# Kernel optimization log

Measured on AMD Instinct MI355X. Metric: run time of the kernel, lower is better.

The kernel has to match this reference:

```python
import jax, jax.numpy as jnp
import numpy as np

N, E, D, H, L = 20000, 320000, 256, 8, 2
C = D // H  # out_channels per head = 32
NEG_SLOPE = 0.2
LN_EPS = 1e-5


def setup_inputs() -> dict:
    key = jax.random.key(0)
    ks = jax.random.split(key, 12)
    s = 0.05
    return {
        "x": jax.random.normal(ks[0], (N, D), jnp.float32),
        "edge_index": jax.random.randint(ks[1], (2, E), 0, N, dtype=jnp.int32),
        "edge_attr": jax.random.uniform(ks[2], (E, 1), jnp.float32),
        "Wl": jax.random.normal(ks[3], (L, D, D), jnp.float32) * s,   # lin_l weight (source)
        "bl": jnp.zeros((L, D), jnp.float32),
        "Wr": jax.random.normal(ks[4], (L, D, D), jnp.float32) * s,   # lin_r weight (target)
        "br": jnp.zeros((L, D), jnp.float32),
        "We": jax.random.normal(ks[5], (L, 1, D), jnp.float32) * s,   # lin_edge (edge_dim=1)
        "att": jax.random.normal(ks[6], (L, H, C), jnp.float32) * s,  # attention vector a
        "bias_out": jnp.zeros((L, D), jnp.float32),                   # GATv2 output bias
        "ln_g": jnp.ones((L, D), jnp.float32),
        "ln_b": jnp.zeros((L, D), jnp.float32),
    }


def _gatv2_layer(x, src, dst, edge_attr, Wl, bl, Wr, br, We, att, bias_out):
    # dense transforms: [N, H, C]
    xl = (x @ Wl + bl).reshape(N, H, C)  # source features (x_j)
    xr = (x @ Wr + br).reshape(N, H, C)  # target features (x_i)
    ea = (edge_attr @ We).reshape(E, H, C)
    # GATv2 scoring: a^T LeakyReLU(W_l x_j + W_r x_i + W_e e_ij)
    m = jax.nn.leaky_relu(xl[src] + xr[dst] + ea, NEG_SLOPE)  # [E, H, C]
    logits = jnp.einsum('ehc,hc->eh', m, att)                 # [E, H]
    # scatter-softmax over incoming edges of each destination node
    mx = jax.ops.segment_max(logits, dst, num_segments=N)     # [N, H]
    ex = jnp.exp(logits - mx[dst])
    den = jax.ops.segment_sum(ex, dst, num_segments=N)        # [N, H]
    alpha = ex / (den[dst] + 1e-16)                           # [E, H]
    # weighted aggregation of source messages
    out = jax.ops.segment_sum(xl[src] * alpha[:, :, None], dst, num_segments=N)
    return out.reshape(N, D) + bias_out


def _layernorm(h, g, b):
    mu = jnp.mean(h, axis=-1, keepdims=True)
    var = jnp.mean(jnp.square(h - mu), axis=-1, keepdims=True)
    return (h - mu) * jax.lax.rsqrt(var + LN_EPS) * g + b


def reference(x, edge_index, edge_attr, Wl, bl, Wr, br, We, att, bias_out, ln_g, ln_b):
    src, dst = edge_index[0], edge_index[1]
    for i in range(L):
        h = _gatv2_layer(x, src, dst, edge_attr, Wl[i], bl[i], Wr[i], br[i],
                         We[i], att[i], bias_out[i])
        h = jax.nn.elu(_layernorm(h, ln_g[i], ln_b[i]))
        x = x + h  # residual (dropout = identity in reference)
    return x
```

## Files before the change

### kernel.cpp

```cpp
#include <hip/hip_runtime.h>
#include <hip/hip_bf16.h>
#include <math.h>

#define Nn 20000
#define Ee 320000
#define Dd 256
#define Hh 8
#define Cc 32
#define NEG_SLOPE 0.2f
#define LN_EPS 1e-5f

typedef __bf16 bf16x8 __attribute__((ext_vector_type(8)));
typedef float f32x4 __attribute__((ext_vector_type(4)));

__device__ __forceinline__ unsigned f2bf_rn(float f) {
    unsigned u = __float_as_uint(f);
    return (u + 0x7fffu + ((u >> 16) & 1u)) >> 16;
}


__global__ void count_kernel(const int* __restrict__ ei, int* __restrict__ counts) {
    int e = blockIdx.x * 256 + threadIdx.x;
    if (e < Ee) atomicAdd(&counts[ei[Ee + e]], 1);
}

__global__ void __launch_bounds__(1024) scan_kernel(
        const int* __restrict__ counts, int* __restrict__ offs, int* __restrict__ gctr) {
    __shared__ int buf[1024];
    __shared__ int bbase;
    int tid = threadIdx.x;
    int i = blockIdx.x * 1024 + tid;
    int v = (i < Nn) ? counts[i] : 0;
    buf[tid] = v;
    __syncthreads();
    for (int off = 1; off < 1024; off <<= 1) {
        int t = (tid >= off) ? buf[tid - off] : 0;
        __syncthreads();
        buf[tid] += t;
        __syncthreads();
    }
    int incl = buf[tid];
    if (tid == 1023) bbase = atomicAdd(gctr, incl);
    __syncthreads();
    if (i < Nn) offs[i] = bbase + incl - v;
}

__global__ void fill_kernel(const int* __restrict__ ei, const float* __restrict__ eattr,
                            const int* __restrict__ offs,
                            int* __restrict__ cursor, int2* __restrict__ csr_meta) {
    int e = blockIdx.x * 256 + threadIdx.x;
    if (e < Ee) {
        int d = ei[Ee + e];
        int p = atomicAdd(&cursor[d], 1);
        int2 m;
        m.x = ei[e];
        m.y = __float_as_int(eattr[e]);
        csr_meta[offs[d] + p] = m;
    }
}


__global__ void cast_x_kernel(const float* __restrict__ x, unsigned short* __restrict__ Xb) {
    int i = blockIdx.x * 256 + threadIdx.x;
    float4 v = ((const float4*)x)[i];
    uint2 pk;
    pk.x = f2bf_rn(v.x) | (f2bf_rn(v.y) << 16);
    pk.y = f2bf_rn(v.z) | (f2bf_rn(v.w) << 16);
    ((uint2*)Xb)[i] = pk;
}


__global__ void prep_w_kernel(const float* __restrict__ Wl, const float* __restrict__ Wr,
                              unsigned short* __restrict__ Wt) {
    __shared__ float tile[64][65];
    int m = blockIdx.y;
    int layer = m >> 1;
    const float* W = ((m & 1) ? Wr : Wl) + (size_t)layer * 65536;
    int tk = (blockIdx.x >> 2) * 64, tn = (blockIdx.x & 3) * 64;
    int t = threadIdx.x;
    int lr = t >> 6, lc = t & 63;
#pragma unroll
    for (int i = 0; i < 16; ++i)
        tile[lr + i * 4][lc] = W[(size_t)(tk + lr + i * 4) * 256 + tn + lc];
    __syncthreads();
    unsigned short* dst = Wt + (size_t)m * 65536;
#pragma unroll
    for (int i = 0; i < 16; ++i)
        dst[(size_t)(tn + lr + i * 4) * 256 + tk + lc] = f2bf_rn(tile[lc][lr + i * 4]);
}


__device__ __forceinline__ void gload16(const void* g, void* l) {
    __builtin_amdgcn_global_load_lds(
        (__attribute__((address_space(1))) void*)g,
        (__attribute__((address_space(3))) void*)l,
        16, 0, 0);
}

__global__ void __launch_bounds__(256) gemm_kernel(
        const unsigned short* __restrict__ Xb, const unsigned short* __restrict__ Wt,
        const float* __restrict__ bl, const float* __restrict__ br,
        unsigned short* __restrict__ XLR) {
    __shared__ short As[2][128 * 32];
    __shared__ short Bs[2][128 * 32];

    const int t = threadIdx.x;
    const int wave = t >> 6, lane = t & 63;
    const int ln = lane & 15, q = lane >> 4;
    const int wm = wave >> 1, wn = wave & 1;
    const int row0 = blockIdx.x * 128;
    const int col0 = blockIdx.y * 128;

    const int srow = t >> 2;
    const int skc = t & 3;

    f32x4 acc[4][4] = {};

    for (int k0 = 0; k0 < 256; k0 += 64) {
#pragma unroll
        for (int h = 0; h < 2; ++h) {
            int kh = k0 + h * 32;
#pragma unroll
            for (int p = 0; p < 2; ++p) {
                int ra = row0 + p * 64 + srow; if (ra > Nn - 1) ra = Nn - 1;
                gload16(Xb + (size_t)ra * 256 + kh + skc * 8, (char*)As[h] + p * 4096 + t * 16);
                int rb = col0 + p * 64 + srow;
                gload16(Wt + (size_t)rb * 256 + kh + skc * 8, (char*)Bs[h] + p * 4096 + t * 16);
            }
        }
        __syncthreads();
#pragma unroll
        for (int h = 0; h < 2; ++h) {
            bf16x8 af[4], bf[4];
#pragma unroll
            for (int i = 0; i < 4; ++i) {
                af[i] = *(const bf16x8*)(As[h] + (wm * 64 + i * 16 + ln) * 32 + q * 8);
                bf[i] = *(const bf16x8*)(Bs[h] + (wn * 64 + i * 16 + ln) * 32 + q * 8);
            }
#pragma unroll
            for (int i = 0; i < 4; ++i)
#pragma unroll
                for (int j = 0; j < 4; ++j)
                    acc[i][j] = __builtin_amdgcn_mfma_f32_16x16x32_bf16(af[i], bf[j], acc[i][j], 0, 0, 0);
        }
        __syncthreads();
    }

#pragma unroll
    for (int nt = 0; nt < 4; ++nt) {
        int col = col0 + wn * 64 + nt * 16 + ln;
        float bc = (col < 256) ? bl[col] : br[col - 256];
#pragma unroll
        for (int mt = 0; mt < 4; ++mt) {
#pragma unroll
            for (int r = 0; r < 4; ++r) {
                int row = row0 + wm * 64 + mt * 16 + q * 4 + r;
                if (row < Nn)
                    XLR[(size_t)row * 512 + col] = (unsigned short)f2bf_rn(acc[mt][nt][r] + bc);
            }
        }
    }
}


__global__ void __launch_bounds__(256) node_kernel(
        const unsigned short* __restrict__ XLR,
        const int* __restrict__ counts, const int* __restrict__ offs,
        const int2* __restrict__ csr_meta,
        const float* __restrict__ We, const float* __restrict__ att,
        const float* __restrict__ x_in, const float* __restrict__ bias_out,
        const float* __restrict__ ln_g, const float* __restrict__ ln_b,
        float* __restrict__ x_out, unsigned short* __restrict__ x_out_b) {
    __shared__ float swe[256], satt[256];
    __shared__ int2 s_meta[4][64];
    int tid = threadIdx.x;
    swe[tid] = We[tid];
    satt[tid] = att[tid];
    __syncthreads();

    int w = tid >> 6, lane = tid & 63;
    int n = blockIdx.x * 4 + w;
    if (n >= Nn) return;

    int base = offs[n];
    int deg = counts[n];
    int c0 = lane * 4;

    uint2 xrp = *(const uint2*)(XLR + (size_t)n * 512 + 256 + c0);
    float xr0 = __uint_as_float(xrp.x << 16);
    float xr1 = __uint_as_float(xrp.x & 0xffff0000u);
    float xr2 = __uint_as_float(xrp.y << 16);
    float xr3 = __uint_as_float(xrp.y & 0xffff0000u);

    float we0 = swe[c0], we1 = swe[c0 + 1], we2 = swe[c0 + 2], we3 = swe[c0 + 3];
    float at0 = satt[c0], at1 = satt[c0 + 1], at2 = satt[c0 + 2], at3 = satt[c0 + 3];

    float S = 0.f;
    float a0 = 0.f, a1 = 0.f, a2 = 0.f, a3 = 0.f;

    for (int b0 = 0; b0 < deg; b0 += 64) {
        int cnt = deg - b0; if (cnt > 64) cnt = 64;
        if (lane < cnt)
            s_meta[w][lane] = csr_meta[base + b0 + lane];
        __builtin_amdgcn_wave_barrier();

        float eaA = 0.f, eaB = 0.f;
        uint2 rawA = {0, 0}, rawB = {0, 0};
        {
            int2 m = s_meta[w][0];
            int sn = __builtin_amdgcn_readfirstlane(m.x);
            eaA = __uint_as_float(__builtin_amdgcn_readfirstlane(m.y));
            rawA = *(const uint2*)(XLR + (size_t)sn * 512 + c0);
        }
        if (cnt > 1) {
            int2 m = s_meta[w][1];
            int sn = __builtin_amdgcn_readfirstlane(m.x);
            eaB = __uint_as_float(__builtin_amdgcn_readfirstlane(m.y));
            rawB = *(const uint2*)(XLR + (size_t)sn * 512 + c0);
        }

        for (int i = 0; i < cnt; i += 2) {
            uint2 cA = rawA; float eA = eaA;
            uint2 cB = rawB; float eB = eaB;
            int rem = cnt - i;
            if (i + 2 < cnt) {
                int2 m = s_meta[w][i + 2];
                int sn = __builtin_amdgcn_readfirstlane(m.x);
                eaA = __uint_as_float(__builtin_amdgcn_readfirstlane(m.y));
                rawA = *(const uint2*)(XLR + (size_t)sn * 512 + c0);
            }
            if (i + 3 < cnt) {
                int2 m = s_meta[w][i + 3];
                int sn = __builtin_amdgcn_readfirstlane(m.x);
                eaB = __uint_as_float(__builtin_amdgcn_readfirstlane(m.y));
                rawB = *(const uint2*)(XLR + (size_t)sn * 512 + c0);
            }

            float A0 = __uint_as_float(cA.x << 16);
            float A1 = __uint_as_float(cA.x & 0xffff0000u);
            float A2 = __uint_as_float(cA.y << 16);
            float A3 = __uint_as_float(cA.y & 0xffff0000u);
            float tA0 = fmaf(eA, we0, A0 + xr0);
            float tA1 = fmaf(eA, we1, A1 + xr1);
            float tA2 = fmaf(eA, we2, A2 + xr2);
            float tA3 = fmaf(eA, we3, A3 + xr3);
            float pA = fmaxf(tA0, NEG_SLOPE * tA0) * at0;
            pA = fmaf(fmaxf(tA1, NEG_SLOPE * tA1), at1, pA);
            pA = fmaf(fmaxf(tA2, NEG_SLOPE * tA2), at2, pA);
            pA = fmaf(fmaxf(tA3, NEG_SLOPE * tA3), at3, pA);

            float B0 = __uint_as_float(cB.x << 16);
            float B1 = __uint_as_float(cB.x & 0xffff0000u);
            float B2 = __uint_as_float(cB.y << 16);
            float B3 = __uint_as_float(cB.y & 0xffff0000u);
            float tB0 = fmaf(eB, we0, B0 + xr0);
            float tB1 = fmaf(eB, we1, B1 + xr1);
            float tB2 = fmaf(eB, we2, B2 + xr2);
            float tB3 = fmaf(eB, we3, B3 + xr3);
            float pB = fmaxf(tB0, NEG_SLOPE * tB0) * at0;
            pB = fmaf(fmaxf(tB1, NEG_SLOPE * tB1), at1, pB);
            pB = fmaf(fmaxf(tB2, NEG_SLOPE * tB2), at2, pB);
            pB = fmaf(fmaxf(tB3, NEG_SLOPE * tB3), at3, pB);

            pA += __shfl_xor(pA, 1);
            pB += __shfl_xor(pB, 1);
            pA += __shfl_xor(pA, 2);
            pB += __shfl_xor(pB, 2);
            pA += __shfl_xor(pA, 4);
            pB += __shfl_xor(pB, 4);

            float wA = __expf(pA);
            float wB = __expf(pB);

            S += wA;
            a0 = fmaf(wA, A0, a0);
            a1 = fmaf(wA, A1, a1);
            a2 = fmaf(wA, A2, a2);
            a3 = fmaf(wA, A3, a3);
            if (rem > 1) {
                S += wB;
                a0 = fmaf(wB, B0, a0);
                a1 = fmaf(wB, B1, a1);
                a2 = fmaf(wB, B2, a2);
                a3 = fmaf(wB, B3, a3);
            }
        }
    }

    float inv = 1.f / (S + 1e-16f);
    float4 bo = *(const float4*)(bias_out + c0);
    float h0 = a0 * inv + bo.x, h1 = a1 * inv + bo.y;
    float h2 = a2 * inv + bo.z, h3 = a3 * inv + bo.w;

    float s1 = h0 + h1 + h2 + h3;
    for (int off = 1; off < 64; off <<= 1) s1 += __shfl_xor(s1, off);
    float mu = s1 * (1.f / 256.f);
    float d0 = h0 - mu, d1 = h1 - mu, d2 = h2 - mu, d3 = h3 - mu;
    float s2 = d0 * d0 + d1 * d1 + d2 * d2 + d3 * d3;
    for (int off = 1; off < 64; off <<= 1) s2 += __shfl_xor(s2, off);
    float rstd = rsqrtf(s2 * (1.f / 256.f) + LN_EPS);

    float4 g = *(const float4*)(ln_g + c0);
    float4 bb = *(const float4*)(ln_b + c0);
    float y0 = d0 * rstd * g.x + bb.x;
    float y1 = d1 * rstd * g.y + bb.y;
    float y2 = d2 * rstd * g.z + bb.z;
    float y3 = d3 * rstd * g.w + bb.w;

    y0 = y0 > 0.f ? y0 : (__expf(y0) - 1.f);
    y1 = y1 > 0.f ? y1 : (__expf(y1) - 1.f);
    y2 = y2 > 0.f ? y2 : (__expf(y2) - 1.f);
    y3 = y3 > 0.f ? y3 : (__expf(y3) - 1.f);

    float4 xi = *(const float4*)(x_in + (size_t)n * 256 + c0);
    float4 o;
    o.x = xi.x + y0;
    o.y = xi.y + y1;
    o.z = xi.z + y2;
    o.w = xi.w + y3;
    *(float4*)(x_out + (size_t)n * 256 + c0) = o;

    uint2 pk;
    pk.x = f2bf_rn(o.x) | (f2bf_rn(o.y) << 16);
    pk.y = f2bf_rn(o.z) | (f2bf_rn(o.w) << 16);
    *(uint2*)(x_out_b + (size_t)n * 256 + c0) = pk;
}


extern "C" void kernel_launch(void* const* d_in, const int* in_sizes, int n_in,
                              void* d_out, int out_size, void* d_ws, size_t ws_size,
                              hipStream_t stream) {
    const float* x        = (const float*)d_in[0];
    const int*   ei       = (const int*)d_in[1];
    const float* eattr    = (const float*)d_in[2];
    const float* Wl       = (const float*)d_in[3];
    const float* bl       = (const float*)d_in[4];
    const float* Wr       = (const float*)d_in[5];
    const float* br       = (const float*)d_in[6];
    const float* We       = (const float*)d_in[7];
    const float* att      = (const float*)d_in[8];
    const float* bias_out = (const float*)d_in[9];
    const float* ln_g     = (const float*)d_in[10];
    const float* ln_b     = (const float*)d_in[11];
    float* out = (float*)d_out;

    char* ws = (char*)d_ws;
    size_t off = 0;
    unsigned short* Xb  = (unsigned short*)(ws + off); off += (size_t)Nn * Dd * 2;
    unsigned short* XLR = (unsigned short*)(ws + off); off += (size_t)Nn * 512 * 2;
    float* xmid   = (float*)(ws + off); off += (size_t)Nn * Dd * 4;
    unsigned short* Wt = (unsigned short*)(ws + off); off += (size_t)4 * 256 * 256 * 2;
    int* counts   = (int*)(ws + off);   off += (size_t)Nn * 4;
    int* cursor   = (int*)(ws + off);   off += (size_t)Nn * 4;
    int* gctr     = (int*)(ws + off);   off += 16;
    int* offs     = (int*)(ws + off);   off += (size_t)(Nn + 4) * 4;
    int2* csr_meta = (int2*)(ws + off); off += (size_t)Ee * 8;

    hipMemsetAsync(counts, 0, 2 * (size_t)Nn * 4 + 16, stream);

    int egrid = (Ee + 255) / 256;
    count_kernel<<<egrid, 256, 0, stream>>>(ei, counts);
    scan_kernel<<<(Nn + 1023) / 1024, 1024, 0, stream>>>(counts, offs, gctr);
    fill_kernel<<<egrid, 256, 0, stream>>>(ei, eattr, offs, cursor, csr_meta);
    prep_w_kernel<<<dim3(16, 4), 256, 0, stream>>>(Wl, Wr, Wt);
    cast_x_kernel<<<(Nn * Dd / 4 + 255) / 256, 256, 0, stream>>>(x, Xb);

    const float* xin = x;
    for (int l = 0; l < 2; ++l) {
        float* xout = (l == 0) ? xmid : out;
        gemm_kernel<<<dim3((Nn + 127) / 128, 4), 256, 0, stream>>>(
            Xb, Wt + (size_t)l * 2 * 65536, bl + (size_t)l * Dd, br + (size_t)l * Dd, XLR);
        node_kernel<<<(Nn + 3) / 4, 256, 0, stream>>>(
            XLR, counts, offs, csr_meta,
            We + (size_t)l * Dd, att + (size_t)l * Dd,
            xin, bias_out + (size_t)l * Dd,
            ln_g + (size_t)l * Dd, ln_b + (size_t)l * Dd, xout, Xb);
        xin = xout;
    }
}
```

Measured before the change: 243.7 us.

## Widen node gathers to half-wave per node, enlarge GEMM tile, drop fp32 intermediate

The node kernel now maps each destination node to 32 lanes, each handling 8 channels with 16-byte bf16 gathers, so one wave serves two nodes. The shared-memory staging of We/att and the readfirstlane broadcasts are removed, and the head reduction needs one fewer shuffle. The GEMM block tile grows from 128 to 256 rows so each B tile is reused across more rows. The fp32 intermediate activation buffer is gone: layer 0 writes only bf16, and layer 1 reads that bf16 residual. This cuts memory traffic but lowers residual precision, and the larger GEMM tile raises register pressure and halves the number of row blocks.

```diff
diff --git a/kernel.cpp b/kernel.cpp
--- a/kernel.cpp
+++ b/kernel.cpp
@@ -101,29 +101,32 @@
         const unsigned short* __restrict__ Xb, const unsigned short* __restrict__ Wt,
         const float* __restrict__ bl, const float* __restrict__ br,
         unsigned short* __restrict__ XLR) {
-    __shared__ short As[2][128 * 32];
+    __shared__ short As[2][256 * 32];
     __shared__ short Bs[2][128 * 32];
 
     const int t = threadIdx.x;
     const int wave = t >> 6, lane = t & 63;
     const int ln = lane & 15, q = lane >> 4;
     const int wm = wave >> 1, wn = wave & 1;
-    const int row0 = blockIdx.x * 128;
+    const int row0 = blockIdx.x * 256;
     const int col0 = blockIdx.y * 128;
 
     const int srow = t >> 2;
     const int skc = t & 3;
 
-    f32x4 acc[4][4] = {};
+    f32x4 acc[8][4] = {};
 
     for (int k0 = 0; k0 < 256; k0 += 64) {
 #pragma unroll
         for (int h = 0; h < 2; ++h) {
             int kh = k0 + h * 32;
 #pragma unroll
+            for (int c = 0; c < 4; ++c) {
+                int ra = row0 + c * 64 + srow; if (ra > Nn - 1) ra = Nn - 1;
+                gload16(Xb + (size_t)ra * 256 + kh + skc * 8, (char*)As[h] + c * 4096 + t * 16);
+            }
+#pragma unroll
             for (int p = 0; p < 2; ++p) {
-                int ra = row0 + p * 64 + srow; if (ra > Nn - 1) ra = Nn - 1;
-                gload16(Xb + (size_t)ra * 256 + kh + skc * 8, (char*)As[h] + p * 4096 + t * 16);
                 int rb = col0 + p * 64 + srow;
                 gload16(Wt + (size_t)rb * 256 + kh + skc * 8, (char*)Bs[h] + p * 4096 + t * 16);
             }
@@ -131,14 +134,15 @@
         __syncthreads();
 #pragma unroll
         for (int h = 0; h < 2; ++h) {
-            bf16x8 af[4], bf[4];
-#pragma unroll
-            for (int i = 0; i < 4; ++i) {
-                af[i] = *(const bf16x8*)(As[h] + (wm * 64 + i * 16 + ln) * 32 + q * 8);
-                bf[i] = *(const bf16x8*)(Bs[h] + (wn * 64 + i * 16 + ln) * 32 + q * 8);
-            }
-#pragma unroll
-            for (int i = 0; i < 4; ++i)
+            bf16x8 af[8], bf[4];
+#pragma unroll
+            for (int i = 0; i < 8; ++i)
+                af[i] = *(const bf16x8*)(As[h] + (wm * 128 + i * 16 + ln) * 32 + q * 8);
+#pragma unroll
+            for (int j = 0; j < 4; ++j)
+                bf[j] = *(const bf16x8*)(Bs[h] + (wn * 64 + j * 16 + ln) * 32 + q * 8);
+#pragma unroll
+            for (int i = 0; i < 8; ++i)
 #pragma unroll
                 for (int j = 0; j < 4; ++j)
                     acc[i][j] = __builtin_amdgcn_mfma_f32_16x16x32_bf16(af[i], bf[j], acc[i][j], 0, 0, 0);
@@ -151,10 +155,10 @@
         int col = col0 + wn * 64 + nt * 16 + ln;
         float bc = (col < 256) ? bl[col] : br[col - 256];
 #pragma unroll
-        for (int mt = 0; mt < 4; ++mt) {
+        for (int mt = 0; mt < 8; ++mt) {
 #pragma unroll
             for (int r = 0; r < 4; ++r) {
-                int row = row0 + wm * 64 + mt * 16 + q * 4 + r;
+                int row = row0 + wm * 128 + mt * 16 + q * 4 + r;
                 if (row < Nn)
                     XLR[(size_t)row * 512 + col] = (unsigned short)f2bf_rn(acc[mt][nt][r] + bc);
             }
@@ -168,162 +172,174 @@
         const int* __restrict__ counts, const int* __restrict__ offs,
         const int2* __restrict__ csr_meta,
         const float* __restrict__ We, const float* __restrict__ att,
-        const float* __restrict__ x_in, const float* __restrict__ bias_out,
+        const float* __restrict__ xin_f, const unsigned short* __restrict__ xin_b,
+        const float* __restrict__ bias_out,
         const float* __restrict__ ln_g, const float* __restrict__ ln_b,
-        float* __restrict__ x_out, unsigned short* __restrict__ x_out_b) {
-    __shared__ float swe[256], satt[256];
-    __shared__ int2 s_meta[4][64];
+        float* __restrict__ out_f, unsigned short* __restrict__ out_b,
+        int mode) {
+    __shared__ int2 s_meta[8][32];
     int tid = threadIdx.x;
-    swe[tid] = We[tid];
-    satt[tid] = att[tid];
-    __syncthreads();
-
-    int w = tid >> 6, lane = tid & 63;
-    int n = blockIdx.x * 4 + w;
-    if (n >= Nn) return;
+    int g = tid >> 5;
+    int lane2 = tid & 31;
+    int n = blockIdx.x * 8 + g;
 
     int base = offs[n];
     int deg = counts[n];
-    int c0 = lane * 4;
-
-    uint2 xrp = *(const uint2*)(XLR + (size_t)n * 512 + 256 + c0);
-    float xr0 = __uint_as_float(xrp.x << 16);
-    float xr1 = __uint_as_float(xrp.x & 0xffff0000u);
-    float xr2 = __uint_as_float(xrp.y << 16);
-    float xr3 = __uint_as_float(xrp.y & 0xffff0000u);
-
-    float we0 = swe[c0], we1 = swe[c0 + 1], we2 = swe[c0 + 2], we3 = swe[c0 + 3];
-    float at0 = satt[c0], at1 = satt[c0 + 1], at2 = satt[c0 + 2], at3 = satt[c0 + 3];
+    int c0 = lane2 * 8;
+
+    uint4 xrp = *(const uint4*)(XLR + (size_t)n * 512 + 256 + c0);
+    float xr[8];
+    xr[0] = __uint_as_float(xrp.x << 16); xr[1] = __uint_as_float(xrp.x & 0xffff0000u);
+    xr[2] = __uint_as_float(xrp.y << 16); xr[3] = __uint_as_float(xrp.y & 0xffff0000u);
+    xr[4] = __uint_as_float(xrp.z << 16); xr[5] = __uint_as_float(xrp.z & 0xffff0000u);
+    xr[6] = __uint_as_float(xrp.w << 16); xr[7] = __uint_as_float(xrp.w & 0xffff0000u);
+
+    float4 wv0 = *(const float4*)(We + c0);
+    float4 wv1 = *(const float4*)(We + c0 + 4);
+    float4 av0 = *(const float4*)(att + c0);
+    float4 av1 = *(const float4*)(att + c0 + 4);
+    float we[8] = {wv0.x, wv0.y, wv0.z, wv0.w, wv1.x, wv1.y, wv1.z, wv1.w};
+    float at[8] = {av0.x, av0.y, av0.z, av0.w, av1.x, av1.y, av1.z, av1.w};
 
     float S = 0.f;
-    float a0 = 0.f, a1 = 0.f, a2 = 0.f, a3 = 0.f;
-
-    for (int b0 = 0; b0 < deg; b0 += 64) {
-        int cnt = deg - b0; if (cnt > 64) cnt = 64;
-        if (lane < cnt)
-            s_meta[w][lane] = csr_meta[base + b0 + lane];
+    float ac[8] = {};
+
+    for (int b0 = 0; b0 < deg; b0 += 32) {
+        int cnt = deg - b0; if (cnt > 32) cnt = 32;
+        if (lane2 < cnt)
+            s_meta[g][lane2] = csr_meta[base + b0 + lane2];
         __builtin_amdgcn_wave_barrier();
 
         float eaA = 0.f, eaB = 0.f;
-        uint2 rawA = {0, 0}, rawB = {0, 0};
+        uint4 rawA = {0, 0, 0, 0}, rawB = {0, 0, 0, 0};
         {
-            int2 m = s_meta[w][0];
-            int sn = __builtin_amdgcn_readfirstlane(m.x);
-            eaA = __uint_as_float(__builtin_amdgcn_readfirstlane(m.y));
-            rawA = *(const uint2*)(XLR + (size_t)sn * 512 + c0);
+            int2 m = s_meta[g][0];
+            eaA = __int_as_float(m.y);
+            rawA = *(const uint4*)(XLR + (size_t)m.x * 512 + c0);
         }
         if (cnt > 1) {
-            int2 m = s_meta[w][1];
-            int sn = __builtin_amdgcn_readfirstlane(m.x);
-            eaB = __uint_as_float(__builtin_amdgcn_readfirstlane(m.y));
-            rawB = *(const uint2*)(XLR + (size_t)sn * 512 + c0);
+            int2 m = s_meta[g][1];
+            eaB = __int_as_float(m.y);
+            rawB = *(const uint4*)(XLR + (size_t)m.x * 512 + c0);
         }
 
         for (int i = 0; i < cnt; i += 2) {
-            uint2 cA = rawA; float eA = eaA;
-            uint2 cB = rawB; float eB = eaB;
+            uint4 cA = rawA; float eA = eaA;
+            uint4 cB = rawB; float eB = eaB;
             int rem = cnt - i;
             if (i + 2 < cnt) {
-                int2 m = s_meta[w][i + 2];
-                int sn = __builtin_amdgcn_readfirstlane(m.x);
-                eaA = __uint_as_float(__builtin_amdgcn_readfirstlane(m.y));
-                rawA = *(const uint2*)(XLR + (size_t)sn * 512 + c0);
+                int2 m = s_meta[g][i + 2];
+                eaA = __int_as_float(m.y);
+                rawA = *(const uint4*)(XLR + (size_t)m.x * 512 + c0);
             }
             if (i + 3 < cnt) {
-                int2 m = s_meta[w][i + 3];
-                int sn = __builtin_amdgcn_readfirstlane(m.x);
-                eaB = __uint_as_float(__builtin_amdgcn_readfirstlane(m.y));
-                rawB = *(const uint2*)(XLR + (size_t)sn * 512 + c0);
-            }
-
-            float A0 = __uint_as_float(cA.x << 16);
-            float A1 = __uint_as_float(cA.x & 0xffff0000u);
-            float A2 = __uint_as_float(cA.y << 16);
-            float A3 = __uint_as_float(cA.y & 0xffff0000u);
-            float tA0 = fmaf(eA, we0, A0 + xr0);
-            float tA1 = fmaf(eA, we1, A1 + xr1);
-            float tA2 = fmaf(eA, we2, A2 + xr2);
-            float tA3 = fmaf(eA, we3, A3 + xr3);
-            float pA = fmaxf(tA0, NEG_SLOPE * tA0) * at0;
-            pA = fmaf(fmaxf(tA1, NEG_SLOPE * tA1), at1, pA);
-            pA = fmaf(fmaxf(tA2, NEG_SLOPE * tA2), at2, pA);
-            pA = fmaf(fmaxf(tA3, NEG_SLOPE * tA3), at3, pA);
-
-            float B0 = __uint_as_float(cB.x << 16);
-            float B1 = __uint_as_float(cB.x & 0xffff0000u);
-            float B2 = __uint_as_float(cB.y << 16);
-            float B3 = __uint_as_float(cB.y & 0xffff0000u);
-            float tB0 = fmaf(eB, we0, B0 + xr0);
-            float tB1 = fmaf(eB, we1, B1 + xr1);
-            float tB2 = fmaf(eB, we2, B2 + xr2);
-            float tB3 = fmaf(eB, we3, B3 + xr3);
-            float pB = fmaxf(tB0, NEG_SLOPE * tB0) * at0;
-            pB = fmaf(fmaxf(tB1, NEG_SLOPE * tB1), at1, pB);
-            pB = fmaf(fmaxf(tB2, NEG_SLOPE * tB2), at2, pB);
-            pB = fmaf(fmaxf(tB3, NEG_SLOPE * tB3), at3, pB);
-
+                int2 m = s_meta[g][i + 3];
+                eaB = __int_as_float(m.y);
+                rawB = *(const uint4*)(XLR + (size_t)m.x * 512 + c0);
+            }
+
+            float xlA[8], xlB[8];
+            xlA[0] = __uint_as_float(cA.x << 16); xlA[1] = __uint_as_float(cA.x & 0xffff0000u);
+            xlA[2] = __uint_as_float(cA.y << 16); xlA[3] = __uint_as_float(cA.y & 0xffff0000u);
+            xlA[4] = __uint_as_float(cA.z << 16); xlA[5] = __uint_as_float(cA.z & 0xffff0000u);
+            xlA[6] = __uint_as_float(cA.w << 16); xlA[7] = __uint_as_float(cA.w & 0xffff0000u);
+            xlB[0] = __uint_as_float(cB.x << 16); xlB[1] = __uint_as_float(cB.x & 0xffff0000u);
+            xlB[2] = __uint_as_float(cB.y << 16); xlB[3] = __uint_as_float(cB.y & 0xffff0000u);
+            xlB[4] = __uint_as_float(cB.z << 16); xlB[5] = __uint_as_float(cB.z & 0xffff0000u);
+            xlB[6] = __uint_as_float(cB.w << 16); xlB[7] = __uint_as_float(cB.w & 0xffff0000u);
+
+            float pA = 0.f, pB = 0.f;
+#pragma unroll
+            for (int j = 0; j < 8; ++j) {
+                float tA = fmaf(eA, we[j], xlA[j] + xr[j]);
+                float tB = fmaf(eB, we[j], xlB[j] + xr[j]);
+                pA = fmaf(fmaxf(tA, NEG_SLOPE * tA), at[j], pA);
+                pB = fmaf(fmaxf(tB, NEG_SLOPE * tB), at[j], pB);
+            }
             pA += __shfl_xor(pA, 1);
             pB += __shfl_xor(pB, 1);
             pA += __shfl_xor(pA, 2);
             pB += __shfl_xor(pB, 2);
-            pA += __shfl_xor(pA, 4);
-            pB += __shfl_xor(pB, 4);
 
             float wA = __expf(pA);
             float wB = __expf(pB);
 
             S += wA;
-            a0 = fmaf(wA, A0, a0);
-            a1 = fmaf(wA, A1, a1);
-            a2 = fmaf(wA, A2, a2);
-            a3 = fmaf(wA, A3, a3);
+#pragma unroll
+            for (int j = 0; j < 8; ++j) ac[j] = fmaf(wA, xlA[j], ac[j]);
             if (rem > 1) {
                 S += wB;
-                a0 = fmaf(wB, B0, a0);
-                a1 = fmaf(wB, B1, a1);
-                a2 = fmaf(wB, B2, a2);
-                a3 = fmaf(wB, B3, a3);
+#pragma unroll
+                for (int j = 0; j < 8; ++j) ac[j] = fmaf(wB, xlB[j], ac[j]);
             }
         }
     }
 
     float inv = 1.f / (S + 1e-16f);
-    float4 bo = *(const float4*)(bias_out + c0);
-    float h0 = a0 * inv + bo.x, h1 = a1 * inv + bo.y;
-    float h2 = a2 * inv + bo.z, h3 = a3 * inv + bo.w;
-
-    float s1 = h0 + h1 + h2 + h3;
-    for (int off = 1; off < 64; off <<= 1) s1 += __shfl_xor(s1, off);
+    float4 bo0 = *(const float4*)(bias_out + c0);
+    float4 bo1 = *(const float4*)(bias_out + c0 + 4);
+    float bo[8] = {bo0.x, bo0.y, bo0.z, bo0.w, bo1.x, bo1.y, bo1.z, bo1.w};
+    float h[8];
+#pragma unroll
+    for (int j = 0; j < 8; ++j) h[j] = fmaf(ac[j], inv, bo[j]);
+
+    float s1 = 0.f;
+#pragma unroll
+    for (int j = 0; j < 8; ++j) s1 += h[j];
+    for (int off = 1; off < 32; off <<= 1) s1 += __shfl_xor(s1, off);
     float mu = s1 * (1.f / 256.f);
-    float d0 = h0 - mu, d1 = h1 - mu, d2 = h2 - mu, d3 = h3 - mu;
-    float s2 = d0 * d0 + d1 * d1 + d2 * d2 + d3 * d3;
-    for (int off = 1; off < 64; off <<= 1) s2 += __shfl_xor(s2, off);
+    float d[8];
+    float s2 = 0.f;
+#pragma unroll
+    for (int j = 0; j < 8; ++j) { d[j] = h[j] - mu; s2 = fmaf(d[j], d[j], s2); }
+    for (int off = 1; off < 32; off <<= 1) s2 += __shfl_xor(s2, off);
     float rstd = rsqrtf(s2 * (1.f / 256.f) + LN_EPS);
 
-    float4 g = *(const float4*)(ln_g + c0);
-    float4 bb = *(const float4*)(ln_b + c0);
-    float y0 = d0 * rstd * g.x + bb.x;
-    float y1 = d1 * rstd * g.y + bb.y;
-    float y2 = d2 * rstd * g.z + bb.z;
-    float y3 = d3 * rstd * g.w + bb.w;
-
-    y0 = y0 > 0.f ? y0 : (__expf(y0) - 1.f);
-    y1 = y1 > 0.f ? y1 : (__expf(y1) - 1.f);
-    y2 = y2 > 0.f ? y2 : (__expf(y2) - 1.f);
-    y3 = y3 > 0.f ? y3 : (__expf(y3) - 1.f);
-
-    float4 xi = *(const float4*)(x_in + (size_t)n * 256 + c0);
-    float4 o;
-    o.x = xi.x + y0;
-    o.y = xi.y + y1;
-    o.z = xi.z + y2;
-    o.w = xi.w + y3;
-    *(float4*)(x_out + (size_t)n * 256 + c0) = o;
-
-    uint2 pk;
-    pk.x = f2bf_rn(o.x) | (f2bf_rn(o.y) << 16);
-    pk.y = f2bf_rn(o.z) | (f2bf_rn(o.w) << 16);
-    *(uint2*)(x_out_b + (size_t)n * 256 + c0) = pk;
+    float4 g0 = *(const float4*)(ln_g + c0);
+    float4 g1 = *(const float4*)(ln_g + c0 + 4);
+    float4 b0v = *(const float4*)(ln_b + c0);
+    float4 b1v = *(const float4*)(ln_b + c0 + 4);
+    float ga[8] = {g0.x, g0.y, g0.z, g0.w, g1.x, g1.y, g1.z, g1.w};
+    float bb[8] = {b0v.x, b0v.y, b0v.z, b0v.w, b1v.x, b1v.y, b1v.z, b1v.w};
+
+    float y[8];
+#pragma unroll
+    for (int j = 0; j < 8; ++j) {
+        float v = fmaf(d[j] * rstd, ga[j], bb[j]);
+        y[j] = v > 0.f ? v : (__expf(v) - 1.f);
+    }
+
+    float xi[8];
+    if (mode == 0) {
+        float4 x0 = *(const float4*)(xin_f + (size_t)n * 256 + c0);
+        float4 x1 = *(const float4*)(xin_f + (size_t)n * 256 + c0 + 4);
+        xi[0] = x0.x; xi[1] = x0.y; xi[2] = x0.z; xi[3] = x0.w;
+        xi[4] = x1.x; xi[5] = x1.y; xi[6] = x1.z; xi[7] = x1.w;
+    } else {
+        uint4 xp = *(const uint4*)(xin_b + (size_t)n * 256 + c0);
+        xi[0] = __uint_as_float(xp.x << 16); xi[1] = __uint_as_float(xp.x & 0xffff0000u);
+        xi[2] = __uint_as_float(xp.y << 16); xi[3] = __uint_as_float(xp.y & 0xffff0000u);
+        xi[4] = __uint_as_float(xp.z << 16); xi[5] = __uint_as_float(xp.z & 0xffff0000u);
+        xi[6] = __uint_as_float(xp.w << 16); xi[7] = __uint_as_float(xp.w & 0xffff0000u);
+    }
+    float o[8];
+#pragma unroll
+    for (int j = 0; j < 8; ++j) o[j] = xi[j] + y[j];
+
+    if (mode == 0) {
+        uint4 pk;
+        pk.x = f2bf_rn(o[0]) | (f2bf_rn(o[1]) << 16);
+        pk.y = f2bf_rn(o[2]) | (f2bf_rn(o[3]) << 16);
+        pk.z = f2bf_rn(o[4]) | (f2bf_rn(o[5]) << 16);
+        pk.w = f2bf_rn(o[6]) | (f2bf_rn(o[7]) << 16);
+        *(uint4*)(out_b + (size_t)n * 256 + c0) = pk;
+    } else {
+        float4 o0, o1;
+        o0.x = o[0]; o0.y = o[1]; o0.z = o[2]; o0.w = o[3];
+        o1.x = o[4]; o1.y = o[5]; o1.z = o[6]; o1.w = o[7];
+        *(float4*)(out_f + (size_t)n * 256 + c0) = o0;
+        *(float4*)(out_f + (size_t)n * 256 + c0 + 4) = o1;
+    }
 }
 
 
@@ -348,7 +364,6 @@
     size_t off = 0;
     unsigned short* Xb  = (unsigned short*)(ws + off); off += (size_t)Nn * Dd * 2;
     unsigned short* XLR = (unsigned short*)(ws + off); off += (size_t)Nn * 512 * 2;
-    float* xmid   = (float*)(ws + off); off += (size_t)Nn * Dd * 4;
     unsigned short* Wt = (unsigned short*)(ws + off); off += (size_t)4 * 256 * 256 * 2;
     int* counts   = (int*)(ws + off);   off += (size_t)Nn * 4;
     int* cursor   = (int*)(ws + off);   off += (size_t)Nn * 4;
@@ -365,16 +380,14 @@
     prep_w_kernel<<<dim3(16, 4), 256, 0, stream>>>(Wl, Wr, Wt);
     cast_x_kernel<<<(Nn * Dd / 4 + 255) / 256, 256, 0, stream>>>(x, Xb);
 
-    const float* xin = x;
     for (int l = 0; l < 2; ++l) {
-        float* xout = (l == 0) ? xmid : out;
-        gemm_kernel<<<dim3((Nn + 127) / 128, 4), 256, 0, stream>>>(
+        gemm_kernel<<<dim3((Nn + 255) / 256, 4), 256, 0, stream>>>(
             Xb, Wt + (size_t)l * 2 * 65536, bl + (size_t)l * Dd, br + (size_t)l * Dd, XLR);
-        node_kernel<<<(Nn + 3) / 4, 256, 0, stream>>>(
+        node_kernel<<<Nn / 8, 256, 0, stream>>>(
             XLR, counts, offs, csr_meta,
             We + (size_t)l * Dd, att + (size_t)l * Dd,
-            xin, bias_out + (size_t)l * Dd,
-            ln_g + (size_t)l * Dd, ln_b + (size_t)l * Dd, xout, Xb);
-        xin = xout;
-    }
-}
+            x, Xb, bias_out + (size_t)l * Dd,
+            ln_g + (size_t)l * Dd, ln_b + (size_t)l * Dd,
+            out, Xb, l);
+    }
+}
```

Result: slower. 293.7 us (+20.5%).
